# Optimization experiments

Measured on AMD Instinct MI355X. Metric: run time of the kernel, lower is better.

## Reference

```python
import jax, jax.numpy as jnp
import numpy as np

PATCH_NUMS = (1, 2, 3, 4, 5, 6, 8, 10, 13, 16)
B = 8
NUM_HEADS = 24
HEAD_DIM = 64
C = NUM_HEADS * HEAD_DIM  # 1536
ROPE_BASE = 10000.0


def _position_ids(batch):
    # Mirrors get_position_ids: 2D grid coords per scale, rescaled to the largest grid.
    largest = PATCH_NUMS[-1]
    coords = []
    for pn in PATCH_NUMS:
        g = np.stack(np.meshgrid(np.arange(pn), np.arange(pn), indexing='ij'), axis=-1)
        coords.append((g.astype(np.float64) / pn * largest).reshape(-1, 2))
    pos = np.concatenate(coords, axis=0).astype(np.float32)  # [L, 2]
    return jnp.asarray(np.broadcast_to(pos, (batch,) + pos.shape))


def setup_inputs() -> dict:
    key = jax.random.key(0)
    k0, k1, k2 = jax.random.split(key, 3)
    L = sum(p * p for p in PATCH_NUMS)  # 680
    s = 0.02
    return {
        'x': jax.random.normal(k0, (B, L, C), jnp.float32),
        'pos_ids': _position_ids(B),                                   # [B, L, 2] float coords
        'w_qkv': jax.random.normal(k1, (3 * C, C), jnp.float32) * s,   # fused QKV weight (no bias in Linear)
        'q_bias': jnp.zeros((C,), jnp.float32),                        # learnable q bias
        'v_bias': jnp.zeros((C,), jnp.float32),                        # learnable v bias (k bias is fixed zero)
        'w_o': jax.random.normal(k2, (C, C), jnp.float32) * s,
        'b_o': jnp.zeros((C,), jnp.float32),
    }


def _rope_2d_cos_sin(pos_ids):
    # LlamaRotaryEmbedding (2D): inv_freq over head_dim with step 4; each spatial axis
    # gets head_dim/2 rotary channels laid out as [fx, fx, fy, fy] (rotate-half pairing).
    inv_freq = 1.0 / (ROPE_BASE ** (jnp.arange(0, HEAD_DIM, 4, dtype=jnp.float32) / HEAD_DIM))  # [hd/4]
    f = pos_ids[..., None] * inv_freq                      # [B, L, 2, hd/4]
    f2 = jnp.concatenate([f, f], axis=-1)                  # [B, L, 2, hd/2]
    emb = f2.reshape(f2.shape[0], f2.shape[1], HEAD_DIM)   # [B, L, hd]
    return jnp.cos(emb), jnp.sin(emb)


def _rotate_half(t):
    h = t.shape[-1] // 2
    return jnp.concatenate([-t[..., h:], t[..., :h]], axis=-1)


def reference(x, pos_ids, w_qkv, q_bias, v_bias, w_o, b_o):
    Bb, L, Cc = x.shape
    bias = jnp.concatenate([q_bias, jnp.zeros_like(q_bias), v_bias])  # zero k bias
    qkv = (x @ w_qkv.T + bias).reshape(Bb, L, 3, NUM_HEADS, HEAD_DIM)
    q, k, v = qkv[:, :, 0], qkv[:, :, 1], qkv[:, :, 2]  # bshd

    cos, sin = _rope_2d_cos_sin(pos_ids)                # [B, L, hd]
    cos = cos[:, :, None, :]                            # broadcast over heads (unsqueeze_dim=2)
    sin = sin[:, :, None, :]
    q = q * cos + _rotate_half(q) * sin
    k = k * cos + _rotate_half(k) * sin

    scale = 1.0 / jnp.sqrt(jnp.asarray(HEAD_DIM, jnp.float32))
    scores = jnp.einsum('bshd,bthd->bhst', q, k) * scale  # [B, H, L, L]
    attn = jax.nn.softmax(scores, axis=-1)
    out = jnp.einsum('bhst,bthd->bshd', attn, v).reshape(Bb, L, Cc)
    return out @ w_o.T + b_o
```

## Files before the change

kernel.cpp:

```cpp
#include <hip/hip_runtime.h>
#include <cmath>

typedef _Float16 f16;
typedef _Float16 f16x2 __attribute__((ext_vector_type(2)));
typedef _Float16 f16x4 __attribute__((ext_vector_type(4)));
typedef _Float16 f16x8 __attribute__((ext_vector_type(8)));
typedef float f32x4 __attribute__((ext_vector_type(4)));

namespace {

constexpr int kB = 8;
constexpr int kL = 680;
constexpr int kH = 24;
constexpr int kD = 64;
constexpr int kC = 1536;
constexpr int kM = kB * kL;
constexpr int kN3 = 3 * kC;
constexpr int kNKT = 11;
constexpr int kNQT = 6;

#define ASYNC_CP16(gp, lp)                                          \
  __builtin_amdgcn_global_load_lds(                                 \
      (const __attribute__((address_space(1))) unsigned int*)(gp),  \
      (__attribute__((address_space(3))) unsigned int*)(lp), 16, 0, 0)

__device__ inline int xcd_swizzle(int bid, int nwg) {
  int q = nwg >> 3, r = nwg & 7;
  int x = bid & 7, idx = bid >> 3;
  return (x < r ? x * (q + 1) : r * (q + 1) + (x - r) * q) + idx;
}

__global__ void cvt_f32_f16(const float* __restrict__ in,
                            f16* __restrict__ out, int n) {
  int i = (blockIdx.x * blockDim.x + threadIdx.x) * 4;
  if (i >= n) return;
  float4 v = *reinterpret_cast<const float4*>(&in[i]);
  f16x4 o;
  o[0] = (f16)v.x;
  o[1] = (f16)v.y;
  o[2] = (f16)v.z;
  o[3] = (f16)v.w;
  *reinterpret_cast<f16x4*>(&out[i]) = o;
}

__global__ void build_bias_kernel(const float* __restrict__ qb,
                                  const float* __restrict__ vb,
                                  float* __restrict__ bias) {
  int i = blockIdx.x * blockDim.x + threadIdx.x;
  if (i >= kN3) return;
  float v = 0.0f;
  if (i < kC) v = qb[i];
  else if (i >= 2 * kC) v = vb[i - 2 * kC];
  bias[i] = v;
}

template <typename OutT>
__global__ __launch_bounds__(512, 2) void gemm256_8ph(
    const f16* __restrict__ A, const f16* __restrict__ Bw,
    const float* __restrict__ bias, OutT* __restrict__ Cm,
    int M, int N, int K) {
  constexpr int HALF = 8192;
  constexpr int ABUF = 2 * HALF;
  constexpr int BUF = 2 * ABUF;
  __shared__ __align__(16) f16 sm[2 * BUF];

  const int tid = threadIdx.x;
  const int w = tid >> 6;
  const int lane = tid & 63;
  const int lr = lane & 15;
  const int quad = lane >> 4;
  const int wr = w >> 2;
  const int wc = w & 3;
  const int gx = gridDim.x;
  const int sw = xcd_swizzle(blockIdx.y * gx + blockIdx.x, gx * gridDim.y);
  const int m0 = (sw / gx) * 256;
  const int n0 = (sw % gx) * 256;
  const int NT = K >> 6;

  const f16* aptr[2][2];
  const f16* bptr[2][2];
  int dstoff0 = tid * 8;
  int dstoff1 = (tid + 512) * 8;
#pragma unroll
  for (int h = 0; h < 2; ++h) {
#pragma unroll
    for (int n = 0; n < 2; ++n) {
      int idx = n * 512 + tid;
      int kb = idx >> 7, r = idx & 127;
      int ra = m0 + h * 128 + r;
      if (ra > M - 1) ra = M - 1;
      aptr[h][n] = A + (size_t)ra * K + kb * 8;
      bptr[h][n] = Bw + (size_t)(n0 + h * 128 + r) * K + kb * 8;
    }
  }

  auto stageA = [&](int t, int h, int q) {
    f16* d = &sm[q * BUF + h * HALF];
    ASYNC_CP16(aptr[h][0] + t * 64, &d[dstoff0]);
    ASYNC_CP16(aptr[h][1] + t * 64, &d[dstoff1]);
  };
  auto stageB = [&](int t, int h, int q) {
    f16* d = &sm[q * BUF + ABUF + h * HALF];
    ASYNC_CP16(bptr[h][0] + t * 64, &d[dstoff0]);
    ASYNC_CP16(bptr[h][1] + t * 64, &d[dstoff1]);
  };

  f32x4 acc[8][4];
#pragma unroll
  for (int i = 0; i < 8; ++i)
#pragma unroll
    for (int j = 0; j < 4; ++j)
#pragma unroll
      for (int c = 0; c < 4; ++c) acc[i][j][c] = 0.0f;

  const int bRow0 = (wc & 1) * 64;

  stageA(0, 0, 0);
  stageA(0, 1, 0);
  stageB(0, 0, 0);
  stageB(0, 1, 0);
  stageB(1, 0, 1);
  stageB(1, 1, 1);
  asm volatile("s_waitcnt vmcnt(4)" ::: "memory");
  __builtin_amdgcn_s_barrier();

  const int NIT = NT >> 1;
  for (int itr = 0; itr < NIT; ++itr) {
    const int t0 = itr * 2;
#pragma unroll
    for (int hf = 0; hf < 2; ++hf) {
      const int tcur = t0 + hf;
      const int ta = tcur + 1;
      const int tb = tcur + 2;
      const f16* Aq = &sm[hf * BUF + wr * HALF];
      const f16* Bq = &sm[hf * BUF + ABUF + (wc >> 1) * HALF];
      f16x8 af[4][2], bfA[2][2], bfB[2][2];

#pragma unroll
      for (int i = 0; i < 4; ++i)
#pragma unroll
        for (int s = 0; s < 2; ++s)
          af[i][s] = *reinterpret_cast<const f16x8*>(
              &Aq[(((s * 4 + quad) << 7) + i * 16 + lr) * 8]);
#pragma unroll
      for (int j = 0; j < 2; ++j)
#pragma unroll
        for (int s = 0; s < 2; ++s)
          bfA[j][s] = *reinterpret_cast<const f16x8*>(
              &Bq[(((s * 4 + quad) << 7) + bRow0 + j * 16 + lr) * 8]);
      if (ta < NT) stageA(ta, 0, hf ^ 1);
      __builtin_amdgcn_s_barrier();
      asm volatile("s_waitcnt lgkmcnt(0)" ::: "memory");
      __builtin_amdgcn_s_setprio(1);
#pragma unroll
      for (int s = 0; s < 2; ++s)
#pragma unroll
        for (int i = 0; i < 4; ++i)
#pragma unroll
          for (int j = 0; j < 2; ++j)
            acc[i][j] = __builtin_amdgcn_mfma_f32_16x16x32_f16(
                af[i][s], bfA[j][s], acc[i][j], 0, 0, 0);
      __builtin_amdgcn_s_setprio(0);
      __builtin_amdgcn_s_barrier();

#pragma unroll
      for (int j = 0; j < 2; ++j)
#pragma unroll
        for (int s = 0; s < 2; ++s)
          bfB[j][s] = *reinterpret_cast<const f16x8*>(
              &Bq[(((s * 4 + quad) << 7) + bRow0 + (j + 2) * 16 + lr) * 8]);
      if (ta < NT) stageA(ta, 1, hf ^ 1);
      __builtin_amdgcn_s_barrier();
      asm volatile("s_waitcnt lgkmcnt(0)" ::: "memory");
      __builtin_amdgcn_s_setprio(1);
#pragma unroll
      for (int s = 0; s < 2; ++s)
#pragma unroll
        for (int i = 0; i < 4; ++i)
#pragma unroll
          for (int j = 0; j < 2; ++j)
            acc[i][j + 2] = __builtin_amdgcn_mfma_f32_16x16x32_f16(
                af[i][s], bfB[j][s], acc[i][j + 2], 0, 0, 0);
      __builtin_amdgcn_s_setprio(0);
      __builtin_amdgcn_s_barrier();

#pragma unroll
      for (int i = 0; i < 4; ++i)
#pragma unroll
        for (int s = 0; s < 2; ++s)
          af[i][s] = *reinterpret_cast<const f16x8*>(
              &Aq[(((s * 4 + quad) << 7) + (i + 4) * 16 + lr) * 8]);
      if (tb < NT) stageB(tb, 0, hf);
      __builtin_amdgcn_s_barrier();
      asm volatile("s_waitcnt lgkmcnt(0)" ::: "memory");
      __builtin_amdgcn_s_setprio(1);
#pragma unroll
      for (int s = 0; s < 2; ++s)
#pragma unroll
        for (int i = 0; i < 4; ++i)
#pragma unroll
          for (int j = 0; j < 2; ++j)
            acc[i + 4][j + 2] = __builtin_amdgcn_mfma_f32_16x16x32_f16(
                af[i][s], bfB[j][s], acc[i + 4][j + 2], 0, 0, 0);
      __builtin_amdgcn_s_setprio(0);
      __builtin_amdgcn_s_barrier();

      if (tb < NT) stageB(tb, 1, hf);
      __builtin_amdgcn_s_barrier();
      __builtin_amdgcn_s_setprio(1);
#pragma unroll
      for (int s = 0; s < 2; ++s)
#pragma unroll
        for (int i = 0; i < 4; ++i)
#pragma unroll
          for (int j = 0; j < 2; ++j)
            acc[i + 4][j] = __builtin_amdgcn_mfma_f32_16x16x32_f16(
                af[i][s], bfA[j][s], acc[i + 4][j], 0, 0, 0);
      __builtin_amdgcn_s_setprio(0);
      if (tb < NT)
        asm volatile("s_waitcnt vmcnt(4)" ::: "memory");
      else
        asm volatile("s_waitcnt vmcnt(0)" ::: "memory");
      __builtin_amdgcn_s_barrier();
    }
  }

  float bv[4];
#pragma unroll
  for (int j = 0; j < 4; ++j) bv[j] = bias[n0 + wc * 64 + j * 16 + lr];
#pragma unroll
  for (int i = 0; i < 8; ++i) {
#pragma unroll
    for (int j = 0; j < 4; ++j) {
#pragma unroll
      for (int r = 0; r < 4; ++r) {
        int row = m0 + wr * 128 + i * 16 + quad * 4 + r;
        if (row < M) {
          int col = n0 + wc * 64 + j * 16 + lr;
          Cm[(size_t)row * N + col] = (OutT)(acc[i][j][r] + bv[j]);
        }
      }
    }
  }
}

__global__ void rope_kernel(f16* __restrict__ qkv,
                            const float* __restrict__ pos) {
  int idx = blockIdx.x * blockDim.x + threadIdx.x;
  if (idx >= kM * kH * 32) return;
  int d = idx & 31;
  int rem = idx >> 5;
  int h = rem % kH;
  int bl = rem / kH;
  float p0 = pos[bl * 2 + 0];
  float p1 = pos[bl * 2 + 1];
  float f = exp2f(-(float)(d & 15) * (13.287712379549449f / 16.0f));
  float s0, c0, s1, c1;
  sincosf(p0 * f, &s0, &c0);
  sincosf(p1 * f, &s1, &c1);
  size_t base = (size_t)bl * kN3 + h * kD;
  {
    float t0 = (float)qkv[base + d];
    float t1 = (float)qkv[base + d + 32];
    qkv[base + d] = (f16)(t0 * c0 - t1 * s0);
    qkv[base + d + 32] = (f16)(t1 * c1 + t0 * s1);
  }
  {
    size_t kb = base + kC;
    float t0 = (float)qkv[kb + d];
    float t1 = (float)qkv[kb + d + 32];
    qkv[kb + d] = (f16)(t0 * c0 - t1 * s0);
    qkv[kb + d + 32] = (f16)(t1 * c1 + t0 * s1);
  }
}

__global__ __launch_bounds__(256, 3) void attn_mfma(
    const f16* __restrict__ qkv, f16* __restrict__ attnout) {
  __shared__ __align__(16) f16 Ks[64 * 72];
  __shared__ __align__(16) f16 Vts[64 * 72];
  __shared__ __align__(16) f16 Pl[4][32 * 72];

  const int tid = threadIdx.x;
  const int w = tid >> 6;
  const int lane = tid & 63;
  const int lr = lane & 15;
  const int qd = lane >> 4;

  const int bid = blockIdx.x;
  const int xcd = bid & 7;
  const int rest = bid >> 3;
  const int qt = rest % kNQT;
  const int g = xcd + 8 * (rest / kNQT);
  const int h = g % kH;
  const int b = g / kH;
  const int q0 = qt * 128;

  f16x8 aq[2][2];
#pragma unroll
  for (int rt = 0; rt < 2; ++rt) {
    int qrow = q0 + w * 32 + rt * 16 + lr;
    if (qrow > kL - 1) qrow = kL - 1;
    const f16* qp = qkv + (size_t)(b * kL + qrow) * kN3 + h * kD;
#pragma unroll
    for (int ks = 0; ks < 2; ++ks)
      aq[rt][ks] =
          *reinterpret_cast<const f16x8*>(qp + ks * 32 + qd * 8);
  }

  const int kkey0 = tid >> 3, kdc = tid & 7;
  const int kkey1 = (tid + 256) >> 3;
  const int vkey0 = (tid & 31) * 2;
  const int vd0 = (tid >> 5) * 8;

  f16x8 kpre0, kpre1, vpre0, vpre1;
  auto prefetch = [&](int kt0) {
    int kg0 = kt0 + kkey0;
    if (kg0 > kL - 1) kg0 = kL - 1;
    kpre0 = *reinterpret_cast<const f16x8*>(
        qkv + (size_t)(b * kL + kg0) * kN3 + kC + h * kD + kdc * 8);
    int kg1 = kt0 + kkey1;
    if (kg1 > kL - 1) kg1 = kL - 1;
    kpre1 = *reinterpret_cast<const f16x8*>(
        qkv + (size_t)(b * kL + kg1) * kN3 + kC + h * kD + kdc * 8);
    int vg0 = kt0 + vkey0;
    if (vg0 > kL - 1) vg0 = kL - 1;
    vpre0 = *reinterpret_cast<const f16x8*>(
        qkv + (size_t)(b * kL + vg0) * kN3 + 2 * kC + h * kD + vd0);
    int vg1 = kt0 + vkey0 + 1;
    if (vg1 > kL - 1) vg1 = kL - 1;
    vpre1 = *reinterpret_cast<const f16x8*>(
        qkv + (size_t)(b * kL + vg1) * kN3 + 2 * kC + h * kD + vd0);
  };
  prefetch(0);

  f32x4 o_acc[2][4];
#pragma unroll
  for (int rt = 0; rt < 2; ++rt)
#pragma unroll
    for (int nt = 0; nt < 4; ++nt)
#pragma unroll
      for (int r = 0; r < 4; ++r) o_acc[rt][nt][r] = 0.0f;
  float lsum[2][4] = {{0.f, 0.f, 0.f, 0.f}, {0.f, 0.f, 0.f, 0.f}};

  for (int it = 0; it < kNKT; ++it) {
    const int kt0 = it * 64;
    __syncthreads();

    *reinterpret_cast<f16x8*>(&Ks[kkey0 * 72 + kdc * 8]) = kpre0;
    *reinterpret_cast<f16x8*>(&Ks[kkey1 * 72 + kdc * 8]) = kpre1;
#pragma unroll
    for (int i = 0; i < 8; ++i) {
      f16x2 pr;
      pr[0] = vpre0[i];
      pr[1] = vpre1[i];
      *reinterpret_cast<f16x2*>(&Vts[(vd0 + i) * 72 + vkey0]) = pr;
    }
    prefetch((it < kNKT - 1) ? (it + 1) * 64 : it * 64);
    __syncthreads();

    f32x4 s_acc[2][4];
#pragma unroll
    for (int rt = 0; rt < 2; ++rt)
#pragma unroll
      for (int t = 0; t < 4; ++t)
#pragma unroll
        for (int r = 0; r < 4; ++r) s_acc[rt][t][r] = 0.0f;
#pragma unroll
    for (int ks = 0; ks < 2; ++ks) {
#pragma unroll
      for (int t = 0; t < 4; ++t) {
        f16x8 bk = *reinterpret_cast<const f16x8*>(
            &Ks[(t * 16 + lr) * 72 + ks * 32 + qd * 8]);
        s_acc[0][t] = __builtin_amdgcn_mfma_f32_16x16x32_f16(
            aq[0][ks], bk, s_acc[0][t], 0, 0, 0);
        s_acc[1][t] = __builtin_amdgcn_mfma_f32_16x16x32_f16(
            aq[1][ks], bk, s_acc[1][t], 0, 0, 0);
      }
    }

#pragma unroll
    for (int rt = 0; rt < 2; ++rt) {
#pragma unroll
      for (int t = 0; t < 4; ++t) {
        const bool valid = (kt0 + t * 16 + lr) < kL;
#pragma unroll
        for (int r = 0; r < 4; ++r) {
          float p = valid ? __expf(s_acc[rt][t][r] * 0.125f) : 0.0f;
          lsum[rt][r] += p;
          Pl[w][(rt * 16 + qd * 4 + r) * 72 + t * 16 + lr] = (f16)p;
        }
      }
    }

#pragma unroll
    for (int ks = 0; ks < 2; ++ks) {
      f16x8 ap[2];
#pragma unroll
      for (int rt = 0; rt < 2; ++rt)
        ap[rt] = *reinterpret_cast<const f16x8*>(
            &Pl[w][(rt * 16 + lr) * 72 + ks * 32 + qd * 8]);
#pragma unroll
      for (int nt = 0; nt < 4; ++nt) {
        f16x8 bv = *reinterpret_cast<const f16x8*>(
            &Vts[(nt * 16 + lr) * 72 + ks * 32 + qd * 8]);
        o_acc[0][nt] = __builtin_amdgcn_mfma_f32_16x16x32_f16(
            ap[0], bv, o_acc[0][nt], 0, 0, 0);
        o_acc[1][nt] = __builtin_amdgcn_mfma_f32_16x16x32_f16(
            ap[1], bv, o_acc[1][nt], 0, 0, 0);
      }
    }
  }

#pragma unroll
  for (int rt = 0; rt < 2; ++rt)
#pragma unroll
    for (int r = 0; r < 4; ++r) {
#pragma unroll
      for (int m = 1; m < 16; m <<= 1)
        lsum[rt][r] += __shfl_xor(lsum[rt][r], m, 64);
    }

#pragma unroll
  for (int rt = 0; rt < 2; ++rt) {
#pragma unroll
    for (int nt = 0; nt < 4; ++nt) {
#pragma unroll
      for (int r = 0; r < 4; ++r) {
        int qr = q0 + w * 32 + rt * 16 + qd * 4 + r;
        if (qr < kL) {
          attnout[(size_t)(b * kL + qr) * kC + h * kD + nt * 16 + lr] =
              (f16)(o_acc[rt][nt][r] / lsum[rt][r]);
        }
      }
    }
  }
}

}

extern "C" void kernel_launch(void* const* d_in, const int* in_sizes, int n_in,
                              void* d_out, int out_size, void* d_ws,
                              size_t ws_size, hipStream_t stream) {
  const float* x = (const float*)d_in[0];
  const float* pos = (const float*)d_in[1];
  const float* w_qkv = (const float*)d_in[2];
  const float* q_bias = (const float*)d_in[3];
  const float* v_bias = (const float*)d_in[4];
  const float* w_o = (const float*)d_in[5];
  const float* b_o = (const float*)d_in[6];
  float* out = (float*)d_out;

  f16* qkv16 = (f16*)d_ws;
  f16* x16 = qkv16 + (size_t)kM * kN3;
  f16* wqkv16 = x16 + (size_t)kM * kC;
  f16* wo16 = wqkv16 + (size_t)kN3 * kC;
  f16* ao16 = wo16 + (size_t)kC * kC;
  float* bias_full = (float*)(ao16 + (size_t)kM * kC);

  cvt_f32_f16<<<(kM * kC / 4 + 255) / 256, 256, 0, stream>>>(x, x16, kM * kC);
  cvt_f32_f16<<<(kN3 * kC / 4 + 255) / 256, 256, 0, stream>>>(w_qkv, wqkv16,
                                                              kN3 * kC);
  cvt_f32_f16<<<(kC * kC / 4 + 255) / 256, 256, 0, stream>>>(w_o, wo16,
                                                             kC * kC);
  build_bias_kernel<<<(kN3 + 255) / 256, 256, 0, stream>>>(q_bias, v_bias,
                                                           bias_full);
  gemm256_8ph<f16><<<dim3(kN3 / 256, (kM + 255) / 256), 512, 0, stream>>>(
      x16, wqkv16, bias_full, qkv16, kM, kN3, kC);
  rope_kernel<<<(kM * kH * 32 + 255) / 256, 256, 0, stream>>>(qkv16, pos);
  attn_mfma<<<dim3(kNQT * kH * kB), 256, 0, stream>>>(qkv16, ao16);
  gemm256_8ph<float><<<dim3(kC / 256, (kM + 255) / 256), 512, 0, stream>>>(
      ao16, wo16, b_o, out, kM, kC, kC);
}
```

Baseline: 402.4 us.

## Fuse RoPE into QKV GEMM epilogue, restructure MFMA fragment order, stripe tile mapping

Removes the standalone RoPE kernel and applies the rotary transform in the QKV GEMM epilogue for Q/K column tiles, computing sin/cos per row from the position ids. This avoids a read-modify-write pass over Q and K. The GEMM inner loop now loads A/B fragments per K-substep (outer-product 4x4 blocks) instead of per column half. A stripe-based tile decode groups blocks four N-tiles wide to improve L2 reuse. The epilogue relies on each wave's 64 columns forming exactly one head, so the d and d+32 pairs sit in the same thread. In exchange it computes sincos redundantly across waves.

```diff
diff --git a/kernel.cpp b/kernel.cpp
--- a/kernel.cpp
+++ b/kernel.cpp
@@ -28,6 +28,19 @@
   int q = nwg >> 3, r = nwg & 7;
   int x = bid & 7, idx = bid >> 3;
   return (x < r ? x * (q + 1) : r * (q + 1) + (x - r) * q) + idx;
+}
+
+__device__ inline void stripe_decode(int id, int gx, int gy, int& mt,
+                                     int& nt) {
+  const int SW = 4;
+  int nst = (gx + SW - 1) / SW;
+  int s = id / (gy * SW);
+  if (s > nst - 1) s = nst - 1;
+  int rem = id - s * gy * SW;
+  int w = gx - s * SW;
+  if (w > SW) w = SW;
+  mt = rem / w;
+  nt = s * SW + rem % w;
 }
 
 __global__ void cvt_f32_f16(const float* __restrict__ in,
@@ -54,11 +67,11 @@
   bias[i] = v;
 }
 
-template <typename OutT>
+template <typename OutT, bool ROPE>
 __global__ __launch_bounds__(512, 2) void gemm256_8ph(
     const f16* __restrict__ A, const f16* __restrict__ Bw,
     const float* __restrict__ bias, OutT* __restrict__ Cm,
-    int M, int N, int K) {
+    const float* __restrict__ pos, int M, int N, int K) {
   constexpr int HALF = 8192;
   constexpr int ABUF = 2 * HALF;
   constexpr int BUF = 2 * ABUF;
@@ -73,8 +86,10 @@
   const int wc = w & 3;
   const int gx = gridDim.x;
   const int sw = xcd_swizzle(blockIdx.y * gx + blockIdx.x, gx * gridDim.y);
-  const int m0 = (sw / gx) * 256;
-  const int n0 = (sw % gx) * 256;
+  int mt, nt;
+  stripe_decode(sw, gx, gridDim.y, mt, nt);
+  const int m0 = mt * 256;
+  const int n0 = nt * 256;
   const int NT = K >> 6;
 
   const f16* aptr[2][2];
@@ -134,88 +149,81 @@
       const int tb = tcur + 2;
       const f16* Aq = &sm[hf * BUF + wr * HALF];
       const f16* Bq = &sm[hf * BUF + ABUF + (wc >> 1) * HALF];
-      f16x8 af[4][2], bfA[2][2], bfB[2][2];
-
-#pragma unroll
-      for (int i = 0; i < 4; ++i)
-#pragma unroll
-        for (int s = 0; s < 2; ++s)
-          af[i][s] = *reinterpret_cast<const f16x8*>(
-              &Aq[(((s * 4 + quad) << 7) + i * 16 + lr) * 8]);
-#pragma unroll
-      for (int j = 0; j < 2; ++j)
-#pragma unroll
-        for (int s = 0; s < 2; ++s)
-          bfA[j][s] = *reinterpret_cast<const f16x8*>(
-              &Bq[(((s * 4 + quad) << 7) + bRow0 + j * 16 + lr) * 8]);
+      f16x8 a0[4], a1[4], b0[4], b1[4];
+
+#pragma unroll
+      for (int i = 0; i < 4; ++i)
+        a0[i] = *reinterpret_cast<const f16x8*>(
+            &Aq[((quad << 7) + i * 16 + lr) * 8]);
+#pragma unroll
+      for (int j = 0; j < 4; ++j)
+        b0[j] = *reinterpret_cast<const f16x8*>(
+            &Bq[((quad << 7) + bRow0 + j * 16 + lr) * 8]);
       if (ta < NT) stageA(ta, 0, hf ^ 1);
       __builtin_amdgcn_s_barrier();
       asm volatile("s_waitcnt lgkmcnt(0)" ::: "memory");
       __builtin_amdgcn_s_setprio(1);
 #pragma unroll
-      for (int s = 0; s < 2; ++s)
-#pragma unroll
-        for (int i = 0; i < 4; ++i)
-#pragma unroll
-          for (int j = 0; j < 2; ++j)
-            acc[i][j] = __builtin_amdgcn_mfma_f32_16x16x32_f16(
-                af[i][s], bfA[j][s], acc[i][j], 0, 0, 0);
+      for (int i = 0; i < 4; ++i)
+#pragma unroll
+        for (int j = 0; j < 4; ++j)
+          acc[i][j] = __builtin_amdgcn_mfma_f32_16x16x32_f16(
+              a0[i], b0[j], acc[i][j], 0, 0, 0);
       __builtin_amdgcn_s_setprio(0);
       __builtin_amdgcn_s_barrier();
 
 #pragma unroll
-      for (int j = 0; j < 2; ++j)
-#pragma unroll
-        for (int s = 0; s < 2; ++s)
-          bfB[j][s] = *reinterpret_cast<const f16x8*>(
-              &Bq[(((s * 4 + quad) << 7) + bRow0 + (j + 2) * 16 + lr) * 8]);
+      for (int j = 0; j < 4; ++j)
+        b1[j] = *reinterpret_cast<const f16x8*>(
+            &Bq[(((4 + quad) << 7) + bRow0 + j * 16 + lr) * 8]);
+#pragma unroll
+      for (int i = 0; i < 4; ++i)
+        a1[i] = *reinterpret_cast<const f16x8*>(
+            &Aq[((quad << 7) + (i + 4) * 16 + lr) * 8]);
       if (ta < NT) stageA(ta, 1, hf ^ 1);
       __builtin_amdgcn_s_barrier();
       asm volatile("s_waitcnt lgkmcnt(0)" ::: "memory");
       __builtin_amdgcn_s_setprio(1);
 #pragma unroll
-      for (int s = 0; s < 2; ++s)
-#pragma unroll
-        for (int i = 0; i < 4; ++i)
-#pragma unroll
-          for (int j = 0; j < 2; ++j)
-            acc[i][j + 2] = __builtin_amdgcn_mfma_f32_16x16x32_f16(
-                af[i][s], bfB[j][s], acc[i][j + 2], 0, 0, 0);
+      for (int i = 0; i < 4; ++i)
+#pragma unroll
+        for (int j = 0; j < 4; ++j)
+          acc[i + 4][j] = __builtin_amdgcn_mfma_f32_16x16x32_f16(
+              a1[i], b0[j], acc[i + 4][j], 0, 0, 0);
       __builtin_amdgcn_s_setprio(0);
       __builtin_amdgcn_s_barrier();
 
 #pragma unroll
       for (int i = 0; i < 4; ++i)
-#pragma unroll
-        for (int s = 0; s < 2; ++s)
-          af[i][s] = *reinterpret_cast<const f16x8*>(
-              &Aq[(((s * 4 + quad) << 7) + (i + 4) * 16 + lr) * 8]);
+        a0[i] = *reinterpret_cast<const f16x8*>(
+            &Aq[(((4 + quad) << 7) + i * 16 + lr) * 8]);
       if (tb < NT) stageB(tb, 0, hf);
       __builtin_amdgcn_s_barrier();
       asm volatile("s_waitcnt lgkmcnt(0)" ::: "memory");
       __builtin_amdgcn_s_setprio(1);
 #pragma unroll
-      for (int s = 0; s < 2; ++s)
-#pragma unroll
-        for (int i = 0; i < 4; ++i)
-#pragma unroll
-          for (int j = 0; j < 2; ++j)
-            acc[i + 4][j + 2] = __builtin_amdgcn_mfma_f32_16x16x32_f16(
-                af[i][s], bfB[j][s], acc[i + 4][j + 2], 0, 0, 0);
+      for (int i = 0; i < 4; ++i)
+#pragma unroll
+        for (int j = 0; j < 4; ++j)
+          acc[i][j] = __builtin_amdgcn_mfma_f32_16x16x32_f16(
+              a0[i], b1[j], acc[i][j], 0, 0, 0);
       __builtin_amdgcn_s_setprio(0);
       __builtin_amdgcn_s_barrier();
 
+#pragma unroll
+      for (int i = 0; i < 4; ++i)
+        a1[i] = *reinterpret_cast<const f16x8*>(
+            &Aq[(((4 + quad) << 7) + (i + 4) * 16 + lr) * 8]);
       if (tb < NT) stageB(tb, 1, hf);
       __builtin_amdgcn_s_barrier();
+      asm volatile("s_waitcnt lgkmcnt(0)" ::: "memory");
       __builtin_amdgcn_s_setprio(1);
 #pragma unroll
-      for (int s = 0; s < 2; ++s)
-#pragma unroll
-        for (int i = 0; i < 4; ++i)
-#pragma unroll
-          for (int j = 0; j < 2; ++j)
-            acc[i + 4][j] = __builtin_amdgcn_mfma_f32_16x16x32_f16(
-                af[i][s], bfA[j][s], acc[i + 4][j], 0, 0, 0);
+      for (int i = 0; i < 4; ++i)
+#pragma unroll
+        for (int j = 0; j < 4; ++j)
+          acc[i + 4][j] = __builtin_amdgcn_mfma_f32_16x16x32_f16(
+              a1[i], b1[j], acc[i + 4][j], 0, 0, 0);
       __builtin_amdgcn_s_setprio(0);
       if (tb < NT)
         asm volatile("s_waitcnt vmcnt(4)" ::: "memory");
@@ -228,49 +236,46 @@
   float bv[4];
 #pragma unroll
   for (int j = 0; j < 4; ++j) bv[j] = bias[n0 + wc * 64 + j * 16 + lr];
-#pragma unroll
-  for (int i = 0; i < 8; ++i) {
-#pragma unroll
-    for (int j = 0; j < 4; ++j) {
+
+  if (ROPE && n0 < 2 * kC) {
+    const float fr = exp2f(-(float)lr * (13.287712379549449f / 16.0f));
+#pragma unroll
+    for (int i = 0; i < 8; ++i) {
 #pragma unroll
       for (int r = 0; r < 4; ++r) {
         int row = m0 + wr * 128 + i * 16 + quad * 4 + r;
         if (row < M) {
-          int col = n0 + wc * 64 + j * 16 + lr;
-          Cm[(size_t)row * N + col] = (OutT)(acc[i][j][r] + bv[j]);
+          float p0 = pos[row * 2 + 0];
+          float p1 = pos[row * 2 + 1];
+          float s0, c0, s1, c1;
+          sincosf(p0 * fr, &s0, &c0);
+          sincosf(p1 * fr, &s1, &c1);
+#pragma unroll
+          for (int j = 0; j < 2; ++j) {
+            float v0 = acc[i][j][r] + bv[j];
+            float v1 = acc[i][j + 2][r] + bv[j + 2];
+            int col = n0 + wc * 64 + j * 16 + lr;
+            Cm[(size_t)row * N + col] = (OutT)(v0 * c0 - v1 * s0);
+            Cm[(size_t)row * N + col + 32] = (OutT)(v1 * c1 + v0 * s1);
+          }
         }
       }
     }
-  }
-}
-
-__global__ void rope_kernel(f16* __restrict__ qkv,
-                            const float* __restrict__ pos) {
-  int idx = blockIdx.x * blockDim.x + threadIdx.x;
-  if (idx >= kM * kH * 32) return;
-  int d = idx & 31;
-  int rem = idx >> 5;
-  int h = rem % kH;
-  int bl = rem / kH;
-  float p0 = pos[bl * 2 + 0];
-  float p1 = pos[bl * 2 + 1];
-  float f = exp2f(-(float)(d & 15) * (13.287712379549449f / 16.0f));
-  float s0, c0, s1, c1;
-  sincosf(p0 * f, &s0, &c0);
-  sincosf(p1 * f, &s1, &c1);
-  size_t base = (size_t)bl * kN3 + h * kD;
-  {
-    float t0 = (float)qkv[base + d];
-    float t1 = (float)qkv[base + d + 32];
-    qkv[base + d] = (f16)(t0 * c0 - t1 * s0);
-    qkv[base + d + 32] = (f16)(t1 * c1 + t0 * s1);
-  }
-  {
-    size_t kb = base + kC;
-    float t0 = (float)qkv[kb + d];
-    float t1 = (float)qkv[kb + d + 32];
-    qkv[kb + d] = (f16)(t0 * c0 - t1 * s0);
-    qkv[kb + d + 32] = (f16)(t1 * c1 + t0 * s1);
+  } else {
+#pragma unroll
+    for (int i = 0; i < 8; ++i) {
+#pragma unroll
+      for (int j = 0; j < 4; ++j) {
+#pragma unroll
+        for (int r = 0; r < 4; ++r) {
+          int row = m0 + wr * 128 + i * 16 + quad * 4 + r;
+          if (row < M) {
+            int col = n0 + wc * 64 + j * 16 + lr;
+            Cm[(size_t)row * N + col] = (OutT)(acc[i][j][r] + bv[j]);
+          }
+        }
+      }
+    }
   }
 }
 
@@ -464,10 +469,11 @@
                                                              kC * kC);
   build_bias_kernel<<<(kN3 + 255) / 256, 256, 0, stream>>>(q_bias, v_bias,
                                                            bias_full);
-  gemm256_8ph<f16><<<dim3(kN3 / 256, (kM + 255) / 256), 512, 0, stream>>>(
-      x16, wqkv16, bias_full, qkv16, kM, kN3, kC);
-  rope_kernel<<<(kM * kH * 32 + 255) / 256, 256, 0, stream>>>(qkv16, pos);
+  gemm256_8ph<f16, true><<<dim3(kN3 / 256, (kM + 255) / 256), 512, 0,
+                           stream>>>(x16, wqkv16, bias_full, qkv16, pos, kM,
+                                     kN3, kC);
   attn_mfma<<<dim3(kNQT * kH * kB), 256, 0, stream>>>(qkv16, ao16);
-  gemm256_8ph<float><<<dim3(kC / 256, (kM + 255) / 256), 512, 0, stream>>>(
-      ao16, wo16, b_o, out, kM, kC, kC);
-}
+  gemm256_8ph<float, false><<<dim3(kC / 256, (kM + 255) / 256), 512, 0,
+                              stream>>>(ao16, wo16, b_o, out, nullptr, kM, kC,
+                                        kC);
+}
```

Measured after the change: 450.2 us. 1.12x slower.
